# Optimization experiments

Measured on AMD Instinct MI355X. Metric: run time of the kernel, lower is better.

## Reference

```python
import jax, jax.numpy as jnp
import numpy as np
from jax import lax


def conv2d(x, w, b):
    # NCHW valid conv, stride 1 (matches torch Conv2d defaults)
    y = lax.conv_general_dilated(x, w, (1, 1), 'VALID',
                                 dimension_numbers=('NCHW', 'OIHW', 'NCHW'))
    return y + b[None, :, None, None]


def maxpool2(x):
    return lax.reduce_window(x, -jnp.inf, lax.max, (1, 1, 2, 2), (1, 1, 2, 2), 'VALID')


def affine_grid(theta, H, W):
    # F.affine_grid(theta, size, align_corners=True): base coords linspace(-1,1)
    xs = jnp.linspace(-1.0, 1.0, W, dtype=theta.dtype)
    ys = jnp.linspace(-1.0, 1.0, H, dtype=theta.dtype)
    gy, gx = jnp.meshgrid(ys, xs, indexing='ij')
    base = jnp.stack([gx, gy, jnp.ones_like(gx)], axis=-1)  # [H,W,3]
    return jnp.einsum('bij,hwj->bhwi', theta, base)  # [B,H,W,2] (x,y)


def grid_sample_bilinear(x, grid):
    # F.grid_sample(x, grid, mode='bilinear', padding_mode='zeros', align_corners=True)
    B, C, H, W = x.shape
    ix = (grid[..., 0] + 1.0) * 0.5 * (W - 1)  # [B,H,W]
    iy = (grid[..., 1] + 1.0) * 0.5 * (H - 1)
    x0 = jnp.floor(ix); y0 = jnp.floor(iy)
    x1 = x0 + 1.0;      y1 = y0 + 1.0

    def gather(yc, xc):
        yi = jnp.clip(yc, 0, H - 1).astype(jnp.int32)
        xi = jnp.clip(xc, 0, W - 1).astype(jnp.int32)
        # per-batch advanced-index gather -> [B,C,Hg,Wg]
        return jax.vmap(lambda img, yy, xx: img[:, yy, xx])(x, yi, xi)

    def valid(yc, xc):
        return ((xc >= 0) & (xc <= W - 1) & (yc >= 0) & (yc <= H - 1)).astype(x.dtype)

    w00 = (x1 - ix) * (y1 - iy)
    w01 = (ix - x0) * (y1 - iy)
    w10 = (x1 - ix) * (iy - y0)
    w11 = (ix - x0) * (iy - y0)
    out = (gather(y0, x0) * (w00 * valid(y0, x0))[:, None]
           + gather(y0, x1) * (w01 * valid(y0, x1))[:, None]
           + gather(y1, x0) * (w10 * valid(y1, x0))[:, None]
           + gather(y1, x1) * (w11 * valid(y1, x1))[:, None])
    return out


def setup_inputs() -> dict:
    key = jax.random.key(0)
    ks = jax.random.split(key, 8)
    B, C, H, W = 128, 3, 224, 224
    LOC_SIZE = 10 * 52 * 52  # 27040, from conv/pool arithmetic on 224x224
    x = jax.random.normal(ks[0], (B, C, H, W), dtype=jnp.float32)
    conv1_w = jax.random.normal(ks[1], (8, C, 7, 7), dtype=jnp.float32) * (1.0 / np.sqrt(C * 49))
    conv1_b = jnp.zeros((8,), dtype=jnp.float32)
    conv2_w = jax.random.normal(ks[2], (10, 8, 5, 5), dtype=jnp.float32) * (1.0 / np.sqrt(8 * 25))
    conv2_b = jnp.zeros((10,), dtype=jnp.float32)
    fc1_w = jax.random.normal(ks[3], (32, LOC_SIZE), dtype=jnp.float32) * (1.0 / np.sqrt(LOC_SIZE))
    fc1_b = jnp.zeros((32,), dtype=jnp.float32)
    fc2_w = jax.random.normal(ks[4], (6, 32), dtype=jnp.float32) * 0.01
    fc2_b = jnp.array([1.0, 0.0, 0.0, 0.0, 1.0, 0.0], dtype=jnp.float32)
    return {"x": x, "conv1_w": conv1_w, "conv1_b": conv1_b,
            "conv2_w": conv2_w, "conv2_b": conv2_b,
            "fc1_w": fc1_w, "fc1_b": fc1_b, "fc2_w": fc2_w, "fc2_b": fc2_b}


def reference(x, conv1_w, conv1_b, conv2_w, conv2_b, fc1_w, fc1_b, fc2_w, fc2_b):
    B, C, H, W = x.shape
    # localization net
    xs = jax.nn.relu(maxpool2(conv2d(x, conv1_w, conv1_b)))
    xs = jax.nn.relu(maxpool2(conv2d(xs, conv2_w, conv2_b)))
    xs = xs.reshape(B, -1)  # [B, 27040]
    h = jax.nn.relu(xs @ fc1_w.T + fc1_b)
    theta = (h @ fc2_w.T + fc2_b).reshape(-1, 2, 3)
    grid = affine_grid(theta, H, W)
    return grid_sample_bilinear(x, grid)
```

## Files before the change

### kernel.cpp

```cpp
#include <hip/hip_runtime.h>
#include <hip/hip_bf16.h>
#include <stdint.h>

typedef __bf16 bf16x8 __attribute__((ext_vector_type(8)));
typedef float f32x4 __attribute__((ext_vector_type(4)));
typedef unsigned long long u64;

union BFrag { uint32_t u[4]; u64 q[2]; bf16x8 v; };

__device__ __forceinline__ void split1(float f, uint32_t& hi, uint32_t& lo) {
  uint32_t b = __float_as_uint(f);
  hi = b >> 16;
  float fl = f - __uint_as_float(b & 0xFFFF0000u);
  lo = __float_as_uint(fl) >> 16;
}

__global__ __launch_bounds__(256) void k0_wprep(
    const float* __restrict__ w1, unsigned short* __restrict__ wpHi,
    unsigned short* __restrict__ wpLo) {
  int id = blockIdx.x * 256 + threadIdx.x;
  if (id >= 4096) return;
  int j = id & 7, n = (id >> 3) & 15, g = (id >> 7) & 3, jf = id >> 9;
  int o = n & 7, half = n >> 3;
  int ky = jf - half, c = j & 3, kx = 2 * g + (j >> 2);
  float f = 0.f;
  if (c < 3 && kx < 7 && ky >= 0 && ky < 7)
    f = w1[o * 147 + c * 49 + ky * 7 + kx];
  uint32_t h, l;
  split1(f, h, l);
  wpHi[id] = (unsigned short)h;
  wpLo[id] = (unsigned short)l;
}

__global__ __launch_bounds__(256) void k0b_wprep(
    const float* __restrict__ w2, unsigned short* __restrict__ wpHi,
    unsigned short* __restrict__ wpLo) {
  int id = blockIdx.x * 256 + threadIdx.x;
  if (id >= 5120) return;
  int j = id & 7, n = (id >> 3) & 15, g = (id >> 7) & 3;
  int hk = id >> 9;
  int h = hk & 1, ky = hk >> 1;
  int c = 4 * h + (j & 3), kx = 2 * g + (j >> 2);
  float f = 0.f;
  if (n < 10 && kx < 5)
    f = w2[n * 200 + c * 25 + ky * 5 + kx];
  uint32_t hh, ll;
  split1(f, hh, ll);
  wpHi[id] = (unsigned short)hh;
  wpLo[id] = (unsigned short)ll;
}

__global__ __launch_bounds__(256) void k1_mfma(
    const float* __restrict__ x, const unsigned short* __restrict__ wpHi,
    const unsigned short* __restrict__ wpLo, const float* __restrict__ bias,
    float* __restrict__ out) {
  __shared__ unsigned short sH[2 * 70 * 24 * 4];
  const int b = blockIdx.z;
  const int x0 = blockIdx.x * 16;
  const int y0blk = blockIdx.y * 64;
  const int tid = threadIdx.x;
  const int lane = tid & 63, wid = tid >> 6;
  const int n = lane & 15, g = lane >> 4;

  BFrag bhi[8], blo[8];
#pragma unroll
  for (int jf = 0; jf < 8; ++jf) {
    uint4 th = *(const uint4*)&wpHi[((jf * 4 + g) * 16 + n) * 8];
    uint4 tl = *(const uint4*)&wpLo[((jf * 4 + g) * 16 + n) * 8];
    bhi[jf].u[0] = th.x; bhi[jf].u[1] = th.y;
    bhi[jf].u[2] = th.z; bhi[jf].u[3] = th.w;
    blo[jf].u[0] = tl.x; blo[jf].u[1] = tl.y;
    blo[jf].u[2] = tl.z; blo[jf].u[3] = tl.w;
  }

  const float* xb = x + (size_t)b * 3 * 50176;
  float pv0[7], pv1[7], pv2[7];
#pragma unroll
  for (int u = 0; u < 7; ++u) {
    int pos = tid + u * 256;
    if (pos < 1680) {
      int row = pos / 24, col = pos % 24;
      int gy = y0blk + row; gy = gy < 223 ? gy : 223;
      int gx = x0 + col;    gx = gx < 223 ? gx : 223;
      const float* p = xb + (size_t)gy * 224 + gx;
      pv0[u] = p[0];
      pv1[u] = p[50176];
      pv2[u] = p[100352];
    }
  }
#pragma unroll
  for (int u = 0; u < 7; ++u) {
    int pos = tid + u * 256;
    if (pos < 1680) {
      uint32_t h0, l0, h1, l1, h2, l2;
      split1(pv0[u], h0, l0);
      split1(pv1[u], h1, l1);
      split1(pv2[u], h2, l2);
      u64 hq = (u64)(h0 | (h1 << 16)) | ((u64)h2 << 32);
      u64 lq = (u64)(l0 | (l1 << 16)) | ((u64)l2 << 32);
      *(u64*)&sH[pos * 4] = hq;
      *(u64*)&sH[6720 + pos * 4] = lq;
    }
  }
  __syncthreads();

  const int y0w = y0blk + wid * 16;
  if (y0w <= 217) {
    f32x4 acc[8];
#pragma unroll
    for (int i = 0; i < 8; ++i) acc[i] = (f32x4){0.f, 0.f, 0.f, 0.f};

    const int mg = n + 2 * g;
    const int rbase = wid * 16;
#pragma unroll
    for (int t = 0; t < 22; ++t) {
      const int s0 = ((rbase + t) * 24 + mg) * 4;
      BFrag ah, al;
      ah.q[0] = *(const u64*)&sH[s0];
      ah.q[1] = *(const u64*)&sH[s0 + 4];
      al.q[0] = *(const u64*)&sH[6720 + s0];
      al.q[1] = *(const u64*)&sH[6720 + s0 + 4];
#pragma unroll
      for (int i = 0; i < 8; ++i) {
        const int jf = t - 2 * i;
        if (jf >= 0 && jf < 8) {
          acc[i] = __builtin_amdgcn_mfma_f32_16x16x32_bf16(ah.v, bhi[jf].v, acc[i], 0, 0, 0);
          acc[i] = __builtin_amdgcn_mfma_f32_16x16x32_bf16(ah.v, blo[jf].v, acc[i], 0, 0, 0);
          acc[i] = __builtin_amdgcn_mfma_f32_16x16x32_bf16(al.v, bhi[jf].v, acc[i], 0, 0, 0);
        }
      }
    }

    const int o = n & 7;
    const float bs = bias[o];
    const int px0 = x0 / 2 + 2 * g;
    const int py0 = y0w / 2;
#pragma unroll
    for (int i = 0; i < 8; ++i) {
      float v0 = fmaxf(acc[i][0], acc[i][1]);
      float v1 = fmaxf(acc[i][2], acc[i][3]);
      float p0 = __shfl_xor(v0, 8, 64);
      float p1 = __shfl_xor(v1, 8, 64);
      const int py = py0 + i;
      if (n < 8 && py < 109) {
        float m0 = fmaxf(v0, p0) + bs;
        float m1 = fmaxf(v1, p1) + bs;
        float* op = out + (((size_t)(b * 109 + py)) * 109 + px0) * 8 + o;
        if (px0 < 109)     op[0] = fmaxf(m0, 0.f);
        if (px0 + 1 < 109) op[8] = fmaxf(m1, 0.f);
      }
    }
  }
}

__global__ __launch_bounds__(128) void k2_mfma(
    const float* __restrict__ in, const unsigned short* __restrict__ wpHi,
    const unsigned short* __restrict__ wpLo, const float* __restrict__ bias,
    float* __restrict__ out) {
  __shared__ unsigned short sH[2 * 20 * 24 * 8];
  const int b = blockIdx.z;
  const int px0 = (blockIdx.x < 6) ? blockIdx.x * 8 : 44;
  const int py0 = (blockIdx.y < 6) ? blockIdx.y * 8 : 44;
  const int x0c = px0 * 2, y0c = py0 * 2;
  const int tid = threadIdx.x;
  const int lane = tid & 63, wid = tid >> 6;
  const int n = lane & 15, g = lane >> 4;

  const float* ib = in + (size_t)b * 109 * 109 * 8;
  float v[4][8];
#pragma unroll
  for (int u = 0; u < 4; ++u) {
    int pos = tid + u * 128;
    if (pos < 480) {
      int row = pos / 24, col = pos % 24;
      int gy = y0c + row;
      int gx = x0c + col; gx = gx < 108 ? gx : 108;
      const float* p = ib + ((size_t)gy * 109 + gx) * 8;
      float4 q0 = *(const float4*)p;
      float4 q1 = *(const float4*)(p + 4);
      v[u][0] = q0.x; v[u][1] = q0.y; v[u][2] = q0.z; v[u][3] = q0.w;
      v[u][4] = q1.x; v[u][5] = q1.y; v[u][6] = q1.z; v[u][7] = q1.w;
    }
  }
#pragma unroll
  for (int u = 0; u < 4; ++u) {
    int pos = tid + u * 128;
    if (pos < 480) {
      uint32_t hh[8], ll[8];
#pragma unroll
      for (int c = 0; c < 8; ++c) split1(v[u][c], hh[c], ll[c]);
      union { uint32_t w[4]; uint4 q; } H, L;
#pragma unroll
      for (int p2 = 0; p2 < 4; ++p2) {
        H.w[p2] = hh[2 * p2] | (hh[2 * p2 + 1] << 16);
        L.w[p2] = ll[2 * p2] | (ll[2 * p2 + 1] << 16);
      }
      *(uint4*)&sH[pos * 8] = H.q;
      *(uint4*)&sH[3840 + pos * 8] = L.q;
    }
  }
  __syncthreads();

  f32x4 acc[8];
#pragma unroll
  for (int i = 0; i < 8; ++i) acc[i] = (f32x4){0.f, 0.f, 0.f, 0.f};

  const int mg = n + 2 * g;
  const int rbase = wid * 8;
#pragma unroll
  for (int h = 0; h < 2; ++h) {
    BFrag bh[5], bl[5];
#pragma unroll
    for (int ky = 0; ky < 5; ++ky) {
      int idx = (((ky * 2 + h) * 4 + g) * 16 + n) * 8;
      uint4 th = *(const uint4*)&wpHi[idx];
      uint4 tl = *(const uint4*)&wpLo[idx];
      bh[ky].u[0] = th.x; bh[ky].u[1] = th.y;
      bh[ky].u[2] = th.z; bh[ky].u[3] = th.w;
      bl[ky].u[0] = tl.x; bl[ky].u[1] = tl.y;
      bl[ky].u[2] = tl.z; bl[ky].u[3] = tl.w;
    }
#pragma unroll
    for (int t = 0; t < 12; ++t) {
      const int s0 = ((rbase + t) * 24 + mg) * 8 + 4 * h;
      BFrag ah, al;
      ah.q[0] = *(const u64*)&sH[s0];
      ah.q[1] = *(const u64*)&sH[s0 + 8];
      al.q[0] = *(const u64*)&sH[3840 + s0];
      al.q[1] = *(const u64*)&sH[3840 + s0 + 8];
#pragma unroll
      for (int ky = 0; ky < 5; ++ky) {
        const int i = t - ky;
        if (i >= 0 && i < 8) {
          acc[i] = __builtin_amdgcn_mfma_f32_16x16x32_bf16(ah.v, bh[ky].v, acc[i], 0, 0, 0);
          acc[i] = __builtin_amdgcn_mfma_f32_16x16x32_bf16(ah.v, bl[ky].v, acc[i], 0, 0, 0);
          acc[i] = __builtin_amdgcn_mfma_f32_16x16x32_bf16(al.v, bh[ky].v, acc[i], 0, 0, 0);
        }
      }
    }
  }

  if (n < 10) {
    const float bs = bias[n];
    const int pxb = px0 + 2 * g;
    const int pyb = py0 + wid * 4;
#pragma unroll
    for (int u = 0; u < 4; ++u) {
      f32x4 A0 = acc[2 * u], A1 = acc[2 * u + 1];
      float m0 = fmaxf(fmaxf(A0[0], A0[1]), fmaxf(A1[0], A1[1])) + bs;
      float m1 = fmaxf(fmaxf(A0[2], A0[3]), fmaxf(A1[2], A1[3])) + bs;
      float* op = out + ((size_t)(b * 10 + n) * 52 + pyb + u) * 52 + pxb;
      op[0] = fmaxf(m0, 0.f);
      op[1] = fmaxf(m1, 0.f);
    }
  }
}

__global__ __launch_bounds__(256) void k3_fc1_partial(
    const float* __restrict__ xs, const float* __restrict__ w,
    float* __restrict__ part) {
  __shared__ float sA[128 * 64];
  __shared__ float sW[64 * 33];
  const int p = blockIdx.x;
  const int tid = threadIdx.x;
  const int n = tid & 31, bg = tid >> 5;
  float acc[16];
#pragma unroll
  for (int i = 0; i < 16; ++i) acc[i] = 0.f;

  for (int ch = 0; ch < 2; ++ch) {
    const int k0 = p * 128 + ch * 64;
    __syncthreads();
#pragma unroll
    for (int bb = 0; bb < 4; ++bb) {
      float v[8];
#pragma unroll
      for (int u = 0; u < 8; ++u) {
        int idx = bb * 2048 + u * 256 + tid;
        int bbv = idx >> 6, k = idx & 63;
        int gk = k0 + k;
        v[u] = (gk < 27040) ? xs[bbv * 27040 + gk] : 0.f;
      }
#pragma unroll
      for (int u = 0; u < 8; ++u) {
        int idx = bb * 2048 + u * 256 + tid;
        sA[idx] = v[u];
      }
    }
    {
      float v[8];
#pragma unroll
      for (int u = 0; u < 8; ++u) {
        int idx = u * 256 + tid;
        int nn = idx >> 6, k = idx & 63;
        int gk = k0 + k;
        v[u] = (gk < 27040) ? w[nn * 27040 + gk] : 0.f;
      }
#pragma unroll
      for (int u = 0; u < 8; ++u) {
        int idx = u * 256 + tid;
        int nn = idx >> 6, k = idx & 63;
        sW[k * 33 + nn] = v[u];
      }
    }
    __syncthreads();
    for (int k = 0; k < 64; k += 4) {
      float w0 = sW[(k + 0) * 33 + n];
      float w1 = sW[(k + 1) * 33 + n];
      float w2 = sW[(k + 2) * 33 + n];
      float w3 = sW[(k + 3) * 33 + n];
#pragma unroll
      for (int i = 0; i < 16; ++i) {
        float4 a = *(const float4*)&sA[(bg * 16 + i) * 64 + k];
        acc[i] = fmaf(a.x, w0, acc[i]);
        acc[i] = fmaf(a.y, w1, acc[i]);
        acc[i] = fmaf(a.z, w2, acc[i]);
        acc[i] = fmaf(a.w, w3, acc[i]);
      }
    }
  }
#pragma unroll
  for (int i = 0; i < 16; ++i)
    part[p * 4096 + (bg * 16 + i) * 32 + n] = acc[i];
}

__global__ __launch_bounds__(256) void k4_reduce(
    const float* __restrict__ part, const float* __restrict__ b1,
    float* __restrict__ h) {
  const int lane = threadIdx.x & 31;
  const int eloc = threadIdx.x >> 5;
  const int e = blockIdx.x * 8 + eloc;
  float s = 0.f;
#pragma unroll
  for (int pc = 0; pc < 8; ++pc) s += part[(pc * 32 + lane) * 4096 + e];
#pragma unroll
  for (int off = 16; off > 0; off >>= 1) s += __shfl_down(s, off, 32);
  if (lane == 0) h[e] = fmaxf(s + b1[e & 31], 0.f);
}

__global__ __launch_bounds__(256) void k5_sample(
    const float* __restrict__ x, const float* __restrict__ h,
    const float* __restrict__ w2, const float* __restrict__ b2,
    float* __restrict__ out) {
  __shared__ float th[6];
  const int b = blockIdx.z;
  if (threadIdx.x < 6) {
    int j = threadIdx.x;
    float s = b2[j];
    for (int m = 0; m < 32; ++m) s = fmaf(h[b * 32 + m], w2[j * 32 + m], s);
    th[j] = s;
  }
  __syncthreads();

  const int pix = blockIdx.x * 256 + threadIdx.x;
  const int hh = pix / 224, ww = pix % 224;
  const float step = 2.0f / 223.0f;
  float gx = ww * step - 1.0f, gy = hh * step - 1.0f;
  float tx = th[0] * gx + th[1] * gy + th[2];
  float ty = th[3] * gx + th[4] * gy + th[5];
  float ix = (tx + 1.0f) * 0.5f * 223.0f;
  float iy = (ty + 1.0f) * 0.5f * 223.0f;
  float x0 = floorf(ix), y0 = floorf(iy);
  float x1 = x0 + 1.f, y1 = y0 + 1.f;
  float wx1 = ix - x0, wx0 = x1 - ix;
  float wy1 = iy - y0, wy0 = y1 - iy;
  float w00 = wx0 * wy0, w01 = wx1 * wy0, w10 = wx0 * wy1, w11 = wx1 * wy1;
  bool vx0 = (x0 >= 0.f) && (x0 <= 223.f);
  bool vx1 = (x1 >= 0.f) && (x1 <= 223.f);
  bool vy0 = (y0 >= 0.f) && (y0 <= 223.f);
  bool vy1 = (y1 >= 0.f) && (y1 <= 223.f);
  w00 = (vx0 && vy0) ? w00 : 0.f;
  w01 = (vx1 && vy0) ? w01 : 0.f;
  w10 = (vx0 && vy1) ? w10 : 0.f;
  w11 = (vx1 && vy1) ? w11 : 0.f;
  int xi0 = (int)fminf(fmaxf(x0, 0.f), 223.f);
  int xi1 = (int)fminf(fmaxf(x1, 0.f), 223.f);
  int yi0 = (int)fminf(fmaxf(y0, 0.f), 223.f);
  int yi1 = (int)fminf(fmaxf(y1, 0.f), 223.f);
#pragma unroll
  for (int c = 0; c < 3; ++c) {
    const float* img = x + (size_t)((b * 3 + c) * 224) * 224;
    float v = img[yi0 * 224 + xi0] * w00 + img[yi0 * 224 + xi1] * w01 +
              img[yi1 * 224 + xi0] * w10 + img[yi1 * 224 + xi1] * w11;
    out[((b * 3 + c) * 224 + hh) * 224 + ww] = v;
  }
}

extern "C" void kernel_launch(void* const* d_in, const int* in_sizes, int n_in,
                              void* d_out, int out_size, void* d_ws,
                              size_t ws_size, hipStream_t stream) {
  const float* x   = (const float*)d_in[0];
  const float* w1  = (const float*)d_in[1];
  const float* b1  = (const float*)d_in[2];
  const float* w2  = (const float*)d_in[3];
  const float* b2  = (const float*)d_in[4];
  const float* fw1 = (const float*)d_in[5];
  const float* fb1 = (const float*)d_in[6];
  const float* fw2 = (const float*)d_in[7];
  const float* fb2 = (const float*)d_in[8];
  float* out = (float*)d_out;

  float* ws   = (float*)d_ws;
  float* out1 = ws;
  float* xs   = out1 + 12166144;
  float* part = xs + 3461120;
  float* hbuf = part + 1048576;
  unsigned short* wpHi  = (unsigned short*)(hbuf + 4096);
  unsigned short* wpLo  = wpHi + 4096;
  unsigned short* wp2Hi = wpLo + 4096;
  unsigned short* wp2Lo = wp2Hi + 5120;

  k0_wprep<<<16, 256, 0, stream>>>(w1, wpHi, wpLo);
  k0b_wprep<<<20, 256, 0, stream>>>(w2, wp2Hi, wp2Lo);
  k1_mfma<<<dim3(14, 4, 128), 256, 0, stream>>>(x, wpHi, wpLo, b1, out1);
  k2_mfma<<<dim3(7, 7, 128), 128, 0, stream>>>(out1, wp2Hi, wp2Lo, b2, xs);
  k3_fc1_partial<<<256, 256, 0, stream>>>(xs, fw1, part);
  k4_reduce<<<512, 256, 0, stream>>>(part, fb1, hbuf);
  k5_sample<<<dim3(196, 1, 128), 256, 0, stream>>>(x, hbuf, fw2, fb2, out);
}
```

Baseline: 209.8 us.

## Widen conv1 tiles to 32 columns with 512-thread blocks and merge weight-prep kernels

The conv1 MFMA kernel now covers a 32-column tile per block, using 8 waves in a 2x4 arrangement, so the halo columns staged in shared memory are amortized over twice as many outputs. The x-tile staging loop is reshaped to match, and the block count along x is halved. Separately, the two weight-prep kernels are fused into a single launch to remove one kernel launch. In exchange, the larger shared-memory footprint and 512-thread blocks may lower the number of resident blocks per CU.

```diff
diff --git a/kernel.cpp b/kernel.cpp
--- a/kernel.cpp
+++ b/kernel.cpp
@@ -16,51 +16,49 @@
 }
 
 __global__ __launch_bounds__(256) void k0_wprep(
-    const float* __restrict__ w1, unsigned short* __restrict__ wpHi,
-    unsigned short* __restrict__ wpLo) {
+    const float* __restrict__ w1, const float* __restrict__ w2,
+    unsigned short* __restrict__ wpHi, unsigned short* __restrict__ wpLo,
+    unsigned short* __restrict__ wp2Hi, unsigned short* __restrict__ wp2Lo) {
   int id = blockIdx.x * 256 + threadIdx.x;
-  if (id >= 4096) return;
-  int j = id & 7, n = (id >> 3) & 15, g = (id >> 7) & 3, jf = id >> 9;
-  int o = n & 7, half = n >> 3;
-  int ky = jf - half, c = j & 3, kx = 2 * g + (j >> 2);
-  float f = 0.f;
-  if (c < 3 && kx < 7 && ky >= 0 && ky < 7)
-    f = w1[o * 147 + c * 49 + ky * 7 + kx];
-  uint32_t h, l;
-  split1(f, h, l);
-  wpHi[id] = (unsigned short)h;
-  wpLo[id] = (unsigned short)l;
-}
-
-__global__ __launch_bounds__(256) void k0b_wprep(
-    const float* __restrict__ w2, unsigned short* __restrict__ wpHi,
-    unsigned short* __restrict__ wpLo) {
-  int id = blockIdx.x * 256 + threadIdx.x;
-  if (id >= 5120) return;
-  int j = id & 7, n = (id >> 3) & 15, g = (id >> 7) & 3;
-  int hk = id >> 9;
-  int h = hk & 1, ky = hk >> 1;
-  int c = 4 * h + (j & 3), kx = 2 * g + (j >> 2);
-  float f = 0.f;
-  if (n < 10 && kx < 5)
-    f = w2[n * 200 + c * 25 + ky * 5 + kx];
-  uint32_t hh, ll;
-  split1(f, hh, ll);
-  wpHi[id] = (unsigned short)hh;
-  wpLo[id] = (unsigned short)ll;
-}
-
-__global__ __launch_bounds__(256) void k1_mfma(
+  if (id < 4096) {
+    int j = id & 7, n = (id >> 3) & 15, g = (id >> 7) & 3, jf = id >> 9;
+    int o = n & 7, half = n >> 3;
+    int ky = jf - half, c = j & 3, kx = 2 * g + (j >> 2);
+    float f = 0.f;
+    if (c < 3 && kx < 7 && ky >= 0 && ky < 7)
+      f = w1[o * 147 + c * 49 + ky * 7 + kx];
+    uint32_t h, l;
+    split1(f, h, l);
+    wpHi[id] = (unsigned short)h;
+    wpLo[id] = (unsigned short)l;
+  }
+  if (id < 5120) {
+    int j = id & 7, n = (id >> 3) & 15, g = (id >> 7) & 3;
+    int hk = id >> 9;
+    int h = hk & 1, ky = hk >> 1;
+    int c = 4 * h + (j & 3), kx = 2 * g + (j >> 2);
+    float f = 0.f;
+    if (n < 10 && kx < 5)
+      f = w2[n * 200 + c * 25 + ky * 5 + kx];
+    uint32_t hh, ll;
+    split1(f, hh, ll);
+    wp2Hi[id] = (unsigned short)hh;
+    wp2Lo[id] = (unsigned short)ll;
+  }
+}
+
+__global__ __launch_bounds__(512) void k1_mfma(
     const float* __restrict__ x, const unsigned short* __restrict__ wpHi,
     const unsigned short* __restrict__ wpLo, const float* __restrict__ bias,
     float* __restrict__ out) {
-  __shared__ unsigned short sH[2 * 70 * 24 * 4];
+  __shared__ unsigned short sH[2 * 70 * 40 * 4];
   const int b = blockIdx.z;
-  const int x0 = blockIdx.x * 16;
+  const int x0 = blockIdx.x * 32;
   const int y0blk = blockIdx.y * 64;
   const int tid = threadIdx.x;
   const int lane = tid & 63, wid = tid >> 6;
   const int n = lane & 15, g = lane >> 4;
+  const int xh = wid & 1, yq = wid >> 1;
 
   BFrag bhi[8], blo[8];
 #pragma unroll
@@ -74,12 +72,12 @@
   }
 
   const float* xb = x + (size_t)b * 3 * 50176;
-  float pv0[7], pv1[7], pv2[7];
-#pragma unroll
-  for (int u = 0; u < 7; ++u) {
-    int pos = tid + u * 256;
-    if (pos < 1680) {
-      int row = pos / 24, col = pos % 24;
+  float pv0[6], pv1[6], pv2[6];
+#pragma unroll
+  for (int u = 0; u < 6; ++u) {
+    int pos = tid + u * 512;
+    if (pos < 2800) {
+      int row = pos / 40, col = pos % 40;
       int gy = y0blk + row; gy = gy < 223 ? gy : 223;
       int gx = x0 + col;    gx = gx < 223 ? gx : 223;
       const float* p = xb + (size_t)gy * 224 + gx;
@@ -89,9 +87,9 @@
     }
   }
 #pragma unroll
-  for (int u = 0; u < 7; ++u) {
-    int pos = tid + u * 256;
-    if (pos < 1680) {
+  for (int u = 0; u < 6; ++u) {
+    int pos = tid + u * 512;
+    if (pos < 2800) {
       uint32_t h0, l0, h1, l1, h2, l2;
       split1(pv0[u], h0, l0);
       split1(pv1[u], h1, l1);
@@ -99,27 +97,27 @@
       u64 hq = (u64)(h0 | (h1 << 16)) | ((u64)h2 << 32);
       u64 lq = (u64)(l0 | (l1 << 16)) | ((u64)l2 << 32);
       *(u64*)&sH[pos * 4] = hq;
-      *(u64*)&sH[6720 + pos * 4] = lq;
+      *(u64*)&sH[11200 + pos * 4] = lq;
     }
   }
   __syncthreads();
 
-  const int y0w = y0blk + wid * 16;
+  const int y0w = y0blk + yq * 16;
   if (y0w <= 217) {
     f32x4 acc[8];
 #pragma unroll
     for (int i = 0; i < 8; ++i) acc[i] = (f32x4){0.f, 0.f, 0.f, 0.f};
 
-    const int mg = n + 2 * g;
-    const int rbase = wid * 16;
+    const int mg = xh * 16 + n + 2 * g;
+    const int rbase = yq * 16;
 #pragma unroll
     for (int t = 0; t < 22; ++t) {
-      const int s0 = ((rbase + t) * 24 + mg) * 4;
+      const int s0 = ((rbase + t) * 40 + mg) * 4;
       BFrag ah, al;
       ah.q[0] = *(const u64*)&sH[s0];
       ah.q[1] = *(const u64*)&sH[s0 + 4];
-      al.q[0] = *(const u64*)&sH[6720 + s0];
-      al.q[1] = *(const u64*)&sH[6720 + s0 + 4];
+      al.q[0] = *(const u64*)&sH[11200 + s0];
+      al.q[1] = *(const u64*)&sH[11200 + s0 + 4];
 #pragma unroll
       for (int i = 0; i < 8; ++i) {
         const int jf = t - 2 * i;
@@ -133,7 +131,7 @@
 
     const int o = n & 7;
     const float bs = bias[o];
-    const int px0 = x0 / 2 + 2 * g;
+    const int px0 = x0 / 2 + xh * 8 + 2 * g;
     const int py0 = y0w / 2;
 #pragma unroll
     for (int i = 0; i < 8; ++i) {
@@ -410,9 +408,8 @@
   unsigned short* wp2Hi = wpLo + 4096;
   unsigned short* wp2Lo = wp2Hi + 5120;
 
-  k0_wprep<<<16, 256, 0, stream>>>(w1, wpHi, wpLo);
-  k0b_wprep<<<20, 256, 0, stream>>>(w2, wp2Hi, wp2Lo);
-  k1_mfma<<<dim3(14, 4, 128), 256, 0, stream>>>(x, wpHi, wpLo, b1, out1);
+  k0_wprep<<<20, 256, 0, stream>>>(w1, w2, wpHi, wpLo, wp2Hi, wp2Lo);
+  k1_mfma<<<dim3(7, 4, 128), 512, 0, stream>>>(x, wpHi, wpLo, b1, out1);
   k2_mfma<<<dim3(7, 7, 128), 128, 0, stream>>>(out1, wp2Hi, wp2Lo, b2, xs);
   k3_fc1_partial<<<256, 256, 0, stream>>>(xs, fw1, part);
   k4_reduce<<<512, 256, 0, stream>>>(part, fb1, hbuf);
```

After: 200.2 us. 1.05x faster.
